# Kernel tuning notes

Measured on AMD Instinct MI355X. Metric: run time of the kernel, lower is better.

Reference implementation:

```python
import jax, jax.numpy as jnp
import numpy as np

N_NODES = 100000
N_EDGES = 3200000
D_FEAT = 512
D_HID = 64
D_LAT = 16
N_CLASS = 10
N_FLOW = 10
K_PROP = 10
ALPHA_TELEPORT = 0.1


def setup_inputs() -> dict:
    key = jax.random.key(0)
    ks = jax.random.split(key, 8)
    x = jax.random.normal(ks[0], (N_NODES, D_FEAT), jnp.float32)
    edge_index = jax.random.randint(ks[1], (2, N_EDGES), 0, N_NODES)
    p_c = jax.random.uniform(ks[2], (N_CLASS,), jnp.float32) + 0.1
    p_c = p_c / p_c.sum()
    W1 = jax.random.normal(ks[3], (D_FEAT, D_HID), jnp.float32) / np.sqrt(D_FEAT).astype(np.float32)
    b1 = jnp.zeros((D_HID,), jnp.float32)
    W2 = jax.random.normal(ks[4], (D_HID, D_LAT), jnp.float32) / np.sqrt(D_HID).astype(np.float32)
    b2 = jnp.zeros((D_LAT,), jnp.float32)
    flow_z0 = jax.random.normal(ks[5], (N_FLOW, N_CLASS, D_LAT), jnp.float32) * 0.1
    flow_alpha_prime = jax.random.normal(ks[6], (N_FLOW, N_CLASS, 1), jnp.float32) * 0.1
    flow_beta = jax.random.normal(ks[7], (N_FLOW, N_CLASS, 1), jnp.float32) * 0.1
    return dict(x=x, edge_index=edge_index, p_c=p_c, W1=W1, b1=b1, W2=W2, b2=b2,
                flow_z0=flow_z0, flow_alpha_prime=flow_alpha_prime, flow_beta=flow_beta)


def _batched_radial_log_prob(z, flow_z0, flow_alpha_prime, flow_beta):
    # Per-class batched radial flow (invertible pyro-style parameterization).
    # z: [N, D] -> log_q: [N, C]
    C, D = flow_z0.shape[1], flow_z0.shape[2]
    zz = jnp.broadcast_to(z[None], (C, z.shape[0], D))  # [C, N, D]
    sum_logdet = jnp.zeros((C, z.shape[0]), z.dtype)
    for l in range(flow_z0.shape[0]):  # small fixed number of flow layers
        z0 = flow_z0[l][:, None, :]                               # [C,1,D]
        alpha = jax.nn.softplus(flow_alpha_prime[l])[:, None, :]  # [C,1,1]
        beta_hat = -alpha + jax.nn.softplus(flow_beta[l])[:, None, :]
        dz = zz - z0
        r = jnp.sqrt(jnp.sum(dz * dz, axis=-1, keepdims=True))    # [C,N,1]
        h = 1.0 / (alpha + r)
        bh = beta_hat * h
        zz = zz + bh * dz
        logdet = (D - 1) * jnp.log1p(bh) + jnp.log1p(bh - beta_hat * r * h * h)
        sum_logdet = sum_logdet + logdet[..., 0]
    log_base = -0.5 * jnp.sum(zz * zz, axis=-1) - 0.5 * D * jnp.log(2.0 * jnp.pi)
    return (log_base + sum_logdet).T  # [N, C]


def _appnp(beta_ft, edge_index, n_nodes):
    # APPNP with self loops and symmetric gcn normalization over edge list.
    src = jnp.concatenate([edge_index[0], jnp.arange(n_nodes)])
    dst = jnp.concatenate([edge_index[1], jnp.arange(n_nodes)])
    deg = jax.ops.segment_sum(jnp.ones_like(src, dtype=beta_ft.dtype), dst, num_segments=n_nodes)
    dinv = jnp.where(deg > 0, jax.lax.rsqrt(jnp.maximum(deg, 1.0)), 0.0)
    norm = (dinv[src] * dinv[dst])[:, None]  # [E+N, 1]
    x0 = beta_ft
    b = beta_ft
    for _ in range(K_PROP):
        agg = jax.ops.segment_sum(norm * b[src], dst, num_segments=n_nodes)
        b = (1.0 - ALPHA_TELEPORT) * agg + ALPHA_TELEPORT * x0
    return b


def reference(x, edge_index, p_c, W1, b1, W2, b2, flow_z0, flow_alpha_prime, flow_beta):
    h = jax.nn.relu(x @ W1 + b1)           # input_encoder (dropout inactive at eval)
    z = h @ W2 + b2                        # latent_encoder, [N, D_LAT]
    log_q = _batched_radial_log_prob(z, flow_z0, flow_alpha_prime, flow_beta)
    log_q_per_class = log_q + jnp.log(p_c)[None, :]
    log_scale = 0.5 * D_LAT * jnp.log(4.0 * jnp.pi)  # 'latent-new' evidence scale
    beta_ft = jnp.exp(jnp.clip(log_q_per_class + log_scale, -30.0, 30.0))
    beta = _appnp(beta_ft, edge_index, x.shape[0])
    alpha = 1.0 + beta
    soft = alpha / jnp.sum(alpha, axis=-1, keepdims=True)
    hard = jnp.argmax(soft, axis=-1)
    return hard[:, None], soft
```

## Files before the change

### kernel.cpp

```cpp
#include <hip/hip_runtime.h>
#include <math.h>
#include <limits.h>

#define DF 512
#define DH 64
#define DL 16
#define NC 10
#define NF 10
#define KPROP 10

#define BSH 7
#define BW  (1 << BSH)
#define MAXB 1024
#define TILE 16384

__device__ __forceinline__ float softplus_(float x){
  return fmaxf(x, 0.0f) + log1pf(expf(-fabsf(x)));
}

#define BM 64
#define BN 64
#define BK 32
__global__ __launch_bounds__(256) void k_gemm1z(const float* __restrict__ x,
    const float* __restrict__ W1, const float* __restrict__ b1,
    const float* __restrict__ W2, const float* __restrict__ b2,
    float* __restrict__ z, int N)
{
  __shared__ float smem[2*BK*(BM+4)];
  float (*At)[BM+4] = (float(*)[BM+4])smem;
  float (*Bs)[BN+4] = (float(*)[BN+4])(smem + BK*(BM+4));
  __shared__ float W2s[DH][DL];
  __shared__ float b2s[DL];
  const int tid = threadIdx.x;
  for (int i = tid; i < DH*DL; i += 256) W2s[i>>4][i&15] = W2[i];
  if (tid < DL) b2s[tid] = b2[tid];
  const int tx = tid & 15, ty = tid >> 4;
  const int row0 = blockIdx.x * BM;
  float acc[4][4] = {};
  for (int k0 = 0; k0 < DF; k0 += BK) {
    #pragma unroll
    for (int i = 0; i < 2; ++i) {
      int idx = tid + i*256;
      int r  = idx >> 3;
      int kk = (idx & 7) << 2;
      int row = row0 + r;
      float4 va = make_float4(0.f,0.f,0.f,0.f);
      if (row < N) va = *(const float4*)&x[(size_t)row*DF + k0 + kk];
      At[kk+0][r]=va.x; At[kk+1][r]=va.y; At[kk+2][r]=va.z; At[kk+3][r]=va.w;
      int r2 = idx >> 4;
      int c4 = (idx & 15) << 2;
      float4 vb = *(const float4*)&W1[(size_t)(k0+r2)*DH + c4];
      Bs[r2][c4+0]=vb.x; Bs[r2][c4+1]=vb.y; Bs[r2][c4+2]=vb.z; Bs[r2][c4+3]=vb.w;
    }
    __syncthreads();
    #pragma unroll
    for (int kk = 0; kk < BK; ++kk) {
      float4 av = *(const float4*)&At[kk][ty<<2];
      float4 bv = *(const float4*)&Bs[kk][tx<<2];
      float a4[4]={av.x,av.y,av.z,av.w};
      float b4[4]={bv.x,bv.y,bv.z,bv.w};
      #pragma unroll
      for (int i=0;i<4;++i)
        #pragma unroll
        for (int j=0;j<4;++j) acc[i][j] = fmaf(a4[i], b4[j], acc[i][j]);
    }
    __syncthreads();
  }
  float4 bias = ((const float4*)b1)[tx];
  float bias4[4] = {bias.x, bias.y, bias.z, bias.w};
  float (*hs)[BM+4] = (float(*)[BM+4])smem;
  #pragma unroll
  for (int i=0;i<4;++i){
    #pragma unroll
    for (int j=0;j<4;++j)
      hs[(ty<<2)+i][(tx<<2)+j] = fmaxf(acc[i][j] + bias4[j], 0.0f);
  }
  __syncthreads();
  int row = tid >> 2, lg = tid & 3;
  float4 zacc = ((const float4*)b2s)[lg];
  #pragma unroll 8
  for (int k = 0; k < DH; ++k){
    float hv = hs[row][k];
    float4 wv = *(const float4*)&W2s[k][lg<<2];
    zacc.x = fmaf(hv, wv.x, zacc.x);
    zacc.y = fmaf(hv, wv.y, zacc.y);
    zacc.z = fmaf(hv, wv.z, zacc.z);
    zacc.w = fmaf(hv, wv.w, zacc.w);
  }
  int grow = row0 + row;
  if (grow < N) ((float4*)z)[(size_t)grow*4 + lg] = zacc;
}

__global__ __launch_bounds__(256) void k_flow2(const float* __restrict__ z,
    const float* __restrict__ pc, const float* __restrict__ z0g,
    const float* __restrict__ apg, const float* __restrict__ fbg,
    const float* __restrict__ dinv,
    float* __restrict__ x0, float* __restrict__ c0, float* __restrict__ y0, int N)
{
  __shared__ float z0s[NF][NC][DL];
  __shared__ float alps[NF][NC];
  __shared__ float bhs[NF][NC];
  __shared__ float lpc[NC];
  int tid = threadIdx.x;
  for (int i = tid; i < NF*NC*DL; i += 256)
    z0s[(i>>4)/NC][(i>>4)%NC][i&15] = z0g[i];
  if (tid < NF*NC){
    int l = tid/NC, c = tid%NC;
    float al = softplus_(apg[tid]);
    alps[l][c] = al;
    bhs[l][c]  = -al + softplus_(fbg[tid]);
  }
  if (tid < NC) lpc[tid] = __logf(pc[tid]);
  __syncthreads();

  int idx = blockIdx.x*256 + tid;
  int n = idx >> 4, c = idx & 15;
  if (n >= N) return;
  float dn = dinv[n];
  if (c >= NC){ x0[idx] = 0.f; c0[idx] = 0.f; y0[idx] = 0.f; return; }

  float zz[DL];
  const float4* z4 = (const float4*)z;
  #pragma unroll
  for (int q=0; q<4; ++q){
    float4 v = z4[(size_t)n*4 + q];
    zz[q*4+0]=v.x; zz[q*4+1]=v.y; zz[q*4+2]=v.z; zz[q*4+3]=v.w;
  }
  const float NEGHALFD_LOG2PI = -14.703016531274762f;
  const float LOGSCALE        =  20.248193975754326f;
  float sld = 0.f;
  #pragma unroll 1
  for (int l=0; l<NF; ++l){
    float al = alps[l][c], bhat = bhs[l][c];
    float dz[DL]; float r2 = 0.f;
    #pragma unroll
    for (int d=0; d<DL; ++d){ float t = zz[d] - z0s[l][c][d]; dz[d]=t; r2 = fmaf(t,t,r2); }
    float r  = sqrtf(r2);
    float hh = 1.0f/(al + r);
    float bh = bhat*hh;
    #pragma unroll
    for (int d=0; d<DL; ++d) zz[d] = fmaf(bh, dz[d], zz[d]);
    sld += 15.0f*__logf(1.0f + bh) + __logf(1.0f + bh - bhat*r*hh*hh);
  }
  float q2 = 0.f;
  #pragma unroll
  for (int d=0; d<DL; ++d) q2 = fmaf(zz[d], zz[d], q2);
  float v = -0.5f*q2 + NEGHALFD_LOG2PI + sld + lpc[c] + LOGSCALE;
  v = fminf(fmaxf(v, -30.f), 30.f);
  float xv = __expf(v);
  x0[idx] = xv;
  c0[idx] = dn*xv;
  y0[idx] = 0.1f*dn*xv;
}

__global__ __launch_bounds__(256) void k_bhist(const int* __restrict__ dst,
    int* __restrict__ bCnt, int E, int B)
{
  __shared__ int hh[MAXB];
  int tid = threadIdx.x;
  for (int b = tid; b < B; b += 256) hh[b] = 0;
  __syncthreads();
  for (int i = blockIdx.x*256 + tid; i < E; i += gridDim.x*256)
    atomicAdd(&hh[dst[i] >> BSH], 1);
  __syncthreads();
  for (int b = tid; b < B; b += 256) if (hh[b]) atomicAdd(&bCnt[b], hh[b]);
}

__global__ void k_bscan(const int* __restrict__ bCnt, int* __restrict__ bOff, int B){
  if (blockIdx.x==0 && threadIdx.x==0){
    int run = 0;
    for (int b=0;b<B;++b){ bOff[b]=run; run+=bCnt[b]; }
    bOff[B]=run;
  }
}

__global__ __launch_bounds__(256) void k_bscatter(const int* __restrict__ src,
    const int* __restrict__ dst, const int* __restrict__ bOff,
    int* __restrict__ bCur, int* __restrict__ bp, int E, int B)
{
  __shared__ int hc[MAXB];
  __shared__ int hb[MAXB];
  int tid = threadIdx.x;
  int base = blockIdx.x * TILE;
  int lim  = base + TILE; if (lim > E) lim = E;
  for (int b = tid; b < B; b += 256) hc[b] = 0;
  __syncthreads();
  for (int i = base + tid; i < lim; i += 256)
    atomicAdd(&hc[dst[i] >> BSH], 1);
  __syncthreads();
  for (int b = tid; b < B; b += 256){
    int c = hc[b];
    hb[b] = c ? atomicAdd(&bCur[b], c) : 0;
    hc[b] = 0;
  }
  __syncthreads();
  for (int i = base + tid; i < lim; i += 256){
    int d = dst[i];
    int b = d >> BSH;
    int pos = bOff[b] + hb[b] + atomicAdd(&hc[b], 1);
    bp[pos] = (src[i] << BSH) | (d & (BW-1));
  }
}

__global__ __launch_bounds__(256) void k_bdeg(const int* __restrict__ bp,
    const int* __restrict__ bOff, int* __restrict__ deg, int N)
{
  __shared__ int cur[BW];
  int tid = threadIdx.x;
  int b = blockIdx.x;
  if (tid < BW) cur[tid] = 0;
  __syncthreads();
  int s = bOff[b], e = bOff[b+1];
  for (int i = s + tid; i < e; i += 256)
    atomicAdd(&cur[bp[i] & (BW-1)], 1);
  __syncthreads();
  int node = (b << BSH) + tid;
  if (tid < BW && node < N) deg[node] = cur[tid] + 1;
}

__global__ void k_dinv(const int* __restrict__ deg, float* __restrict__ dinv,
    float* __restrict__ dinv2, int N){
  int n = blockIdx.x*256 + threadIdx.x;
  if (n < N){
    float d = (float)deg[n];
    float dv = 1.0f / sqrtf(d);
    dinv[n]  = dv;
    dinv2[n] = dv*dv;
  }
}

__global__ __launch_bounds__(256) void k_scan_part(const int* __restrict__ deg,
    int* __restrict__ part, int N){
  __shared__ int sd[256];
  int base = blockIdx.x*1024;
  int tid = threadIdx.x;
  int s = 0;
  #pragma unroll
  for (int i=0;i<4;++i){ int idx = base + tid*4 + i; if (idx < N) s += deg[idx]; }
  sd[tid] = s; __syncthreads();
  for (int ofs=128; ofs>0; ofs>>=1){ if (tid<ofs) sd[tid]+=sd[tid+ofs]; __syncthreads(); }
  if (tid==0) part[blockIdx.x] = sd[0];
}

__global__ void k_scan_top(int* part, int nb){
  if (blockIdx.x==0 && threadIdx.x==0){
    int run = 0;
    for (int i=0;i<nb;++i){ int v = part[i]; part[i] = run; run += v; }
  }
}

__global__ __launch_bounds__(256) void k_scan_final(const int* __restrict__ deg,
    const int* __restrict__ part, int* __restrict__ off, int N, int E)
{
  __shared__ int sc[256];
  int base = blockIdx.x*1024;
  int tid = threadIdx.x;
  int v[4]; int s = 0;
  #pragma unroll
  for (int i=0;i<4;++i){ int idx = base + tid*4 + i; v[i] = (idx<N)?deg[idx]:0; s += v[i]; }
  sc[tid] = s; __syncthreads();
  for (int ofs=1; ofs<256; ofs<<=1){
    int t = (tid>=ofs) ? sc[tid-ofs] : 0;
    __syncthreads();
    sc[tid] += t;
    __syncthreads();
  }
  int ex = sc[tid] - s + part[blockIdx.x];
  #pragma unroll
  for (int i=0;i<4;++i){
    int idx = base + tid*4 + i;
    if (idx < N){
      off[idx] = ex;
      if (idx == N-1) off[N] = ex + v[i];
      ex += v[i];
    }
  }
}

__global__ __launch_bounds__(256) void k_place(const int* __restrict__ bp,
    const int* __restrict__ bOff, const int* __restrict__ off,
    int* __restrict__ csr, int N)
{
  __shared__ int cur[BW];
  int tid = threadIdx.x;
  int b = blockIdx.x;
  int node0 = b << BSH;
  if (tid < BW){
    cur[tid] = 1;
    int node = node0 + tid;
    if (node < N) csr[off[node]] = node;
  }
  __syncthreads();
  int s = bOff[b], e = bOff[b+1];
  for (int i = s + tid; i < e; i += 256){
    int v  = bp[i];
    int dl = v & (BW-1);
    int sn = v >> BSH;
    int d  = node0 + dl;
    int p  = off[d] + atomicAdd(&cur[dl], 1);
    csr[p] = sn;
  }
}

__global__ __launch_bounds__(256) void k_rank(int* __restrict__ csr,
    const int* __restrict__ off, int N)
{
  int wid  = (blockIdx.x*256 + threadIdx.x) >> 6;
  int lane = threadIdx.x & 63;
  if (wid >= N) return;
  int s = off[wid], e = off[wid+1];
  int d = e - s;
  if (d <= 1) return;
  if (d <= 64){
    int v = (lane < d) ? csr[s+lane] : INT_MAX;
    int rank = 0;
    for (int j = 0; j < d; ++j){
      int bv = __shfl(v, j);
      rank += (bv < v) || (bv == v && j < lane);
    }
    if (lane < d) csr[s+rank] = v;
  } else if (d <= 256){
    int v0 = (lane      < d) ? csr[s+lane      ] : INT_MAX;
    int v1 = (lane+64   < d) ? csr[s+lane+64   ] : INT_MAX;
    int v2 = (lane+128  < d) ? csr[s+lane+128  ] : INT_MAX;
    int v3 = (lane+192  < d) ? csr[s+lane+192  ] : INT_MAX;
    int r0=0,r1=0,r2=0,r3=0;
    for (int j = 0; j < d; ++j){
      int slot = j >> 6, jl = j & 63;
      int bv = (slot==0) ? __shfl(v0,jl) : (slot==1) ? __shfl(v1,jl)
             : (slot==2) ? __shfl(v2,jl) : __shfl(v3,jl);
      r0 += (bv < v0) || (bv == v0 && j < lane);
      r1 += (bv < v1) || (bv == v1 && j < lane+64);
      r2 += (bv < v2) || (bv == v2 && j < lane+128);
      r3 += (bv < v3) || (bv == v3 && j < lane+192);
    }
    if (lane      < d) csr[s+r0]=v0;
    if (lane+64   < d) csr[s+r1]=v1;
    if (lane+128  < d) csr[s+r2]=v2;
    if (lane+192  < d) csr[s+r3]=v3;
  } else {
    if (lane == 0){
      for (int i = s+1; i < e; ++i){
        int key = csr[i]; int j = i-1;
        while (j >= s && csr[j] > key){ csr[j+1] = csr[j]; --j; }
        csr[j+1] = key;
      }
    }
  }
}

__global__ __launch_bounds__(256) void k_prop(const float* __restrict__ cin,
    const float* __restrict__ y0, const float* __restrict__ dinv2,
    float* __restrict__ cout,
    const int* __restrict__ csr, const int* __restrict__ off, int N)
{
  int t = blockIdx.x*256 + threadIdx.x;
  int n = t >> 2, q = t & 3;
  if (n >= N) return;
  const float4* c4 = (const float4*)cin;
  float4 a0 = make_float4(0.f,0.f,0.f,0.f);
  float4 a1 = make_float4(0.f,0.f,0.f,0.f);
  float4 a2 = make_float4(0.f,0.f,0.f,0.f);
  float4 a3 = make_float4(0.f,0.f,0.f,0.f);
  int s = off[n], e = off[n+1];
  int i = s;
  for (; i+4 <= e; i += 4){
    int s0 = csr[i], s1 = csr[i+1], s2 = csr[i+2], s3 = csr[i+3];
    float4 v0 = c4[(size_t)s0*4 + q];
    float4 v1 = c4[(size_t)s1*4 + q];
    float4 v2 = c4[(size_t)s2*4 + q];
    float4 v3 = c4[(size_t)s3*4 + q];
    a0.x += v0.x; a0.y += v0.y; a0.z += v0.z; a0.w += v0.w;
    a1.x += v1.x; a1.y += v1.y; a1.z += v1.z; a1.w += v1.w;
    a2.x += v2.x; a2.y += v2.y; a2.z += v2.z; a2.w += v2.w;
    a3.x += v3.x; a3.y += v3.y; a3.z += v3.z; a3.w += v3.w;
  }
  for (; i < e; ++i){
    float4 v0 = c4[(size_t)csr[i]*4 + q];
    a0.x += v0.x; a0.y += v0.y; a0.z += v0.z; a0.w += v0.w;
  }
  float w9 = 0.9f * dinv2[n];
  float4 yv = ((const float4*)y0)[(size_t)n*4 + q];
  float4 o;
  o.x = fmaf(w9, (a0.x+a1.x)+(a2.x+a3.x), yv.x);
  o.y = fmaf(w9, (a0.y+a1.y)+(a2.y+a3.y), yv.y);
  o.z = fmaf(w9, (a0.z+a1.z)+(a2.z+a3.z), yv.z);
  o.w = fmaf(w9, (a0.w+a1.w)+(a2.w+a3.w), yv.w);
  ((float4*)cout)[(size_t)n*4 + q] = o;
}

__global__ __launch_bounds__(256) void k_prop_final(const float* __restrict__ cin,
    const float* __restrict__ x0, const float* __restrict__ dinv,
    const int* __restrict__ csr, const int* __restrict__ off,
    float* __restrict__ out, int N)
{
  int t = blockIdx.x*256 + threadIdx.x;
  int n = t >> 2, q = t & 3;
  if (n >= N) return;
  const float4* c4 = (const float4*)cin;
  float4 a0 = make_float4(0.f,0.f,0.f,0.f);
  float4 a1 = make_float4(0.f,0.f,0.f,0.f);
  float4 a2 = make_float4(0.f,0.f,0.f,0.f);
  float4 a3 = make_float4(0.f,0.f,0.f,0.f);
  int s = off[n], e = off[n+1];
  int i = s;
  for (; i+4 <= e; i += 4){
    int s0 = csr[i], s1 = csr[i+1], s2 = csr[i+2], s3 = csr[i+3];
    float4 v0 = c4[(size_t)s0*4 + q];
    float4 v1 = c4[(size_t)s1*4 + q];
    float4 v2 = c4[(size_t)s2*4 + q];
    float4 v3 = c4[(size_t)s3*4 + q];
    a0.x += v0.x; a0.y += v0.y; a0.z += v0.z; a0.w += v0.w;
    a1.x += v1.x; a1.y += v1.y; a1.z += v1.z; a1.w += v1.w;
    a2.x += v2.x; a2.y += v2.y; a2.z += v2.z; a2.w += v2.w;
    a3.x += v3.x; a3.y += v3.y; a3.z += v3.z; a3.w += v3.w;
  }
  for (; i < e; ++i){
    float4 v0 = c4[(size_t)csr[i]*4 + q];
    a0.x += v0.x; a0.y += v0.y; a0.z += v0.z; a0.w += v0.w;
  }
  float w9 = 0.9f * dinv[n];
  float4 xv = ((const float4*)x0)[(size_t)n*4 + q];
  float4 al;
  al.x = fmaf(w9, (a0.x+a1.x)+(a2.x+a3.x), fmaf(0.1f, xv.x, 1.f));
  al.y = fmaf(w9, (a0.y+a1.y)+(a2.y+a3.y), fmaf(0.1f, xv.y, 1.f));
  al.z = fmaf(w9, (a0.z+a1.z)+(a2.z+a3.z), fmaf(0.1f, xv.z, 1.f));
  al.w = fmaf(w9, (a0.w+a1.w)+(a2.w+a3.w), fmaf(0.1f, xv.w, 1.f));

  float sv = 0.f;
  if (q < 2)       sv = al.x + al.y + al.z + al.w;
  else if (q == 2) sv = al.x + al.y;
  sv += __shfl_xor(sv, 1, 4);
  sv += __shfl_xor(sv, 2, 4);

  float bv = -1e30f; int bi = 999;
  int cb = q*4;
  int nvalid = (q < 2) ? 4 : (q == 2 ? 2 : 0);
  float av[4] = {al.x, al.y, al.z, al.w};
  for (int j = 0; j < nvalid; ++j){
    if (av[j] > bv){ bv = av[j]; bi = cb + j; }
  }
  #pragma unroll
  for (int o = 1; o <= 2; o <<= 1){
    float vo = __shfl_xor(bv, o, 4);
    int  io  = __shfl_xor(bi, o, 4);
    if (vo > bv || (vo == bv && io < bi)){ bv = vo; bi = io; }
  }

  float inv = 1.0f / sv;
  size_t sb = (size_t)N + (size_t)n*NC;
  for (int j = 0; j < nvalid; ++j) out[sb + cb + j] = av[j] * inv;
  if (q == 0) out[n] = (float)bi;
}

extern "C" void kernel_launch(void* const* d_in, const int* in_sizes, int n_in,
                              void* d_out, int out_size, void* d_ws, size_t ws_size,
                              hipStream_t stream)
{
  const float* x  = (const float*)d_in[0];
  const int*   ei = (const int*)  d_in[1];
  const float* pc = (const float*)d_in[2];
  const float* W1 = (const float*)d_in[3];
  const float* b1 = (const float*)d_in[4];
  const float* W2 = (const float*)d_in[5];
  const float* b2 = (const float*)d_in[6];
  const float* z0 = (const float*)d_in[7];
  const float* ap = (const float*)d_in[8];
  const float* fb = (const float*)d_in[9];
  float* out = (float*)d_out;

  const int N = in_sizes[0] / DF;
  const int E = in_sizes[1] / 2;
  const int* src = ei;
  const int* dst = ei + E;
  const int B = (N + BW - 1) >> BSH;

  char* ws = (char*)d_ws;
  size_t o = 0;
  size_t region0 = (size_t)E*sizeof(int);
  if ((size_t)N*DL*sizeof(float) > region0) region0 = (size_t)N*DL*sizeof(float);
  int*   bp   = (int*)  (ws + o);
  float* z    = (float*)(ws + o);
  o += region0;
  int*   csr  = (int*)  (ws + o); o += (size_t)(E+N)*sizeof(int);
  float* x0   = (float*)(ws + o); o += (size_t)N*DL*sizeof(float);
  float* c0   = (float*)(ws + o); o += (size_t)N*DL*sizeof(float);
  float* y0   = (float*)(ws + o); o += (size_t)N*DL*sizeof(float);
  float* cA   = (float*)(ws + o); o += (size_t)N*DL*sizeof(float);
  float* cB   = (float*)(ws + o); o += (size_t)N*DL*sizeof(float);
  int*   deg  = (int*)  (ws + o); o += (size_t)N*sizeof(int);
  float* dinv = (float*)(ws + o); o += (size_t)N*sizeof(float);
  float* dinv2= (float*)(ws + o); o += (size_t)N*sizeof(float);
  int*   offs = (int*)  (ws + o); o += (size_t)(N+2)*sizeof(int);
  int*   part = (int*)  (ws + o); o += 4096;
  int*   bCnt = (int*)  (ws + o); o += MAXB*sizeof(int);
  int*   bOff = (int*)  (ws + o); o += (MAXB+1)*sizeof(int);
  int*   bCur = (int*)  (ws + o); o += MAXB*sizeof(int);

  const int TB = 256;
  int gN  = (N + TB - 1) / TB;
  int nb  = (N + 1023) / 1024;

  hipMemsetAsync(bCnt, 0, MAXB*sizeof(int), stream);
  hipMemsetAsync(bCur, 0, MAXB*sizeof(int), stream);
  k_bhist<<<512, TB, 0, stream>>>(dst, bCnt, E, B);
  k_bscan<<<1, 1, 0, stream>>>(bCnt, bOff, B);
  k_bscatter<<<(E + TILE - 1)/TILE, TB, 0, stream>>>(src, dst, bOff, bCur, bp, E, B);
  k_bdeg<<<B, TB, 0, stream>>>(bp, bOff, deg, N);
  k_dinv<<<gN, TB, 0, stream>>>(deg, dinv, dinv2, N);
  k_scan_part<<<nb, TB, 0, stream>>>(deg, part, N);
  k_scan_top<<<1, 1, 0, stream>>>(part, nb);
  k_scan_final<<<nb, TB, 0, stream>>>(deg, part, offs, N, E);
  k_place<<<B, TB, 0, stream>>>(bp, bOff, offs, csr, N);
  k_rank<<<(N + 3) / 4, TB, 0, stream>>>(csr, offs, N);

  k_gemm1z<<<(N + BM - 1) / BM, TB, 0, stream>>>(x, W1, b1, W2, b2, z, N);
  k_flow2<<<((N*DL) + TB - 1) / TB, TB, 0, stream>>>(z, pc, z0, ap, fb, dinv,
                                                     x0, c0, y0, N);

  int gP = ((N*4) + TB - 1) / TB;
  const float* cin = c0;
  for (int it = 0; it < KPROP-1; ++it){
    float* cout = (it & 1) ? cB : cA;
    k_prop<<<gP, TB, 0, stream>>>(cin, y0, dinv2, cout, csr, offs, N);
    cin = cout;
  }
  k_prop_final<<<gP, TB, 0, stream>>>(cin, x0, dinv, csr, offs, out, N);
}
```

Baseline: 776.5 us.

## Split propagation features into two 8-wide halves for cache-friendlier gathers

Splits the 16-wide per-node propagation state into separate low and high 8-float arrays. Each propagation iteration now launches blocks that work on one half at a time, so the gathered working set per pass is half the size and more likely to stay in cache. The gather loop is unrolled to 8 neighbors. The dinv computation is also folded into the degree kernel, removing one launch. The cost is two gather passes over the CSR indices per iteration and more complex indexing.

```diff
diff --git a/kernel.cpp b/kernel.cpp
--- a/kernel.cpp
+++ b/kernel.cpp
@@ -95,7 +95,8 @@
     const float* __restrict__ pc, const float* __restrict__ z0g,
     const float* __restrict__ apg, const float* __restrict__ fbg,
     const float* __restrict__ dinv,
-    float* __restrict__ x0, float* __restrict__ c0, float* __restrict__ y0, int N)
+    float* __restrict__ x0, float* __restrict__ cL, float* __restrict__ cH,
+    float* __restrict__ yL, float* __restrict__ yH, int N)
 {
   __shared__ float z0s[NF][NC][DL];
   __shared__ float alps[NF][NC];
@@ -117,7 +118,12 @@
   int n = idx >> 4, c = idx & 15;
   if (n >= N) return;
   float dn = dinv[n];
-  if (c >= NC){ x0[idx] = 0.f; c0[idx] = 0.f; y0[idx] = 0.f; return; }
+  if (c >= NC){
+    x0[idx] = 0.f;
+    cH[(size_t)n*8 + (c-8)] = 0.f;
+    yH[(size_t)n*8 + (c-8)] = 0.f;
+    return;
+  }
 
   float zz[DL];
   const float4* z4 = (const float4*)z;
@@ -149,8 +155,14 @@
   v = fminf(fmaxf(v, -30.f), 30.f);
   float xv = __expf(v);
   x0[idx] = xv;
-  c0[idx] = dn*xv;
-  y0[idx] = 0.1f*dn*xv;
+  float cv = dn*xv;
+  if (c < 8){
+    cL[(size_t)n*8 + c] = cv;
+    yL[(size_t)n*8 + c] = 0.1f*cv;
+  } else {
+    cH[(size_t)n*8 + (c-8)] = cv;
+    yH[(size_t)n*8 + (c-8)] = 0.1f*cv;
+  }
 }
 
 __global__ __launch_bounds__(256) void k_bhist(const int* __restrict__ dst,
@@ -203,7 +215,8 @@
 }
 
 __global__ __launch_bounds__(256) void k_bdeg(const int* __restrict__ bp,
-    const int* __restrict__ bOff, int* __restrict__ deg, int N)
+    const int* __restrict__ bOff, int* __restrict__ deg,
+    float* __restrict__ dinv, float* __restrict__ dinv2, int N)
 {
   __shared__ int cur[BW];
   int tid = threadIdx.x;
@@ -215,17 +228,12 @@
     atomicAdd(&cur[bp[i] & (BW-1)], 1);
   __syncthreads();
   int node = (b << BSH) + tid;
-  if (tid < BW && node < N) deg[node] = cur[tid] + 1;
-}
-
-__global__ void k_dinv(const int* __restrict__ deg, float* __restrict__ dinv,
-    float* __restrict__ dinv2, int N){
-  int n = blockIdx.x*256 + threadIdx.x;
-  if (n < N){
-    float d = (float)deg[n];
-    float dv = 1.0f / sqrtf(d);
-    dinv[n]  = dv;
-    dinv2[n] = dv*dv;
+  if (tid < BW && node < N){
+    int d = cur[tid] + 1;
+    deg[node] = d;
+    float dv = 1.0f / sqrtf((float)d);
+    dinv[node]  = dv;
+    dinv2[node] = dv*dv;
   }
 }
 
@@ -349,15 +357,82 @@
   }
 }
 
-__global__ __launch_bounds__(256) void k_prop(const float* __restrict__ cin,
-    const float* __restrict__ y0, const float* __restrict__ dinv2,
-    float* __restrict__ cout,
+__global__ __launch_bounds__(256) void k_prop_half(
+    const float* __restrict__ cLin, const float* __restrict__ cHin,
+    const float* __restrict__ yL,  const float* __restrict__ yH,
+    const float* __restrict__ dinv2,
+    float* __restrict__ cLout, float* __restrict__ cHout,
     const int* __restrict__ csr, const int* __restrict__ off, int N)
+{
+  int bid = blockIdx.x;
+  int half = (bid & 7) >> 2;
+  int node_blk = ((bid >> 3) << 2) | (bid & 3);
+  int t = threadIdx.x;
+  int n = node_blk*128 + (t >> 1);
+  int q = t & 1;
+  if (n >= N) return;
+  const float4* cin = (const float4*)(half ? cHin : cLin);
+  const float4* yin = (const float4*)(half ? yH : yL);
+  float4* cout = (float4*)(half ? cHout : cLout);
+
+  float4 a0 = make_float4(0.f,0.f,0.f,0.f);
+  float4 a1 = make_float4(0.f,0.f,0.f,0.f);
+  float4 a2 = make_float4(0.f,0.f,0.f,0.f);
+  float4 a3 = make_float4(0.f,0.f,0.f,0.f);
+  int s = off[n], e = off[n+1];
+  int i = s;
+  for (; i+8 <= e; i += 8){
+    int s0 = csr[i],   s1 = csr[i+1], s2 = csr[i+2], s3 = csr[i+3];
+    int s4 = csr[i+4], s5 = csr[i+5], s6 = csr[i+6], s7 = csr[i+7];
+    float4 v0 = cin[(size_t)s0*2 + q];
+    float4 v1 = cin[(size_t)s1*2 + q];
+    float4 v2 = cin[(size_t)s2*2 + q];
+    float4 v3 = cin[(size_t)s3*2 + q];
+    float4 v4 = cin[(size_t)s4*2 + q];
+    float4 v5 = cin[(size_t)s5*2 + q];
+    float4 v6 = cin[(size_t)s6*2 + q];
+    float4 v7 = cin[(size_t)s7*2 + q];
+    a0.x += v0.x; a0.y += v0.y; a0.z += v0.z; a0.w += v0.w;
+    a1.x += v1.x; a1.y += v1.y; a1.z += v1.z; a1.w += v1.w;
+    a2.x += v2.x; a2.y += v2.y; a2.z += v2.z; a2.w += v2.w;
+    a3.x += v3.x; a3.y += v3.y; a3.z += v3.z; a3.w += v3.w;
+    a0.x += v4.x; a0.y += v4.y; a0.z += v4.z; a0.w += v4.w;
+    a1.x += v5.x; a1.y += v5.y; a1.z += v5.z; a1.w += v5.w;
+    a2.x += v6.x; a2.y += v6.y; a2.z += v6.z; a2.w += v6.w;
+    a3.x += v7.x; a3.y += v7.y; a3.z += v7.z; a3.w += v7.w;
+  }
+  for (; i+2 <= e; i += 2){
+    int s0 = csr[i], s1 = csr[i+1];
+    float4 v0 = cin[(size_t)s0*2 + q];
+    float4 v1 = cin[(size_t)s1*2 + q];
+    a0.x += v0.x; a0.y += v0.y; a0.z += v0.z; a0.w += v0.w;
+    a1.x += v1.x; a1.y += v1.y; a1.z += v1.z; a1.w += v1.w;
+  }
+  if (i < e){
+    float4 v0 = cin[(size_t)csr[i]*2 + q];
+    a0.x += v0.x; a0.y += v0.y; a0.z += v0.z; a0.w += v0.w;
+  }
+  float w9 = 0.9f * dinv2[n];
+  float4 yv = yin[(size_t)n*2 + q];
+  float4 o;
+  o.x = fmaf(w9, (a0.x+a1.x)+(a2.x+a3.x), yv.x);
+  o.y = fmaf(w9, (a0.y+a1.y)+(a2.y+a3.y), yv.y);
+  o.z = fmaf(w9, (a0.z+a1.z)+(a2.z+a3.z), yv.z);
+  o.w = fmaf(w9, (a0.w+a1.w)+(a2.w+a3.w), yv.w);
+  cout[(size_t)n*2 + q] = o;
+}
+
+__global__ __launch_bounds__(256) void k_prop_final(
+    const float* __restrict__ cLin, const float* __restrict__ cHin,
+    const float* __restrict__ x0, const float* __restrict__ dinv,
+    const int* __restrict__ csr, const int* __restrict__ off,
+    float* __restrict__ out, int N)
 {
   int t = blockIdx.x*256 + threadIdx.x;
   int n = t >> 2, q = t & 3;
   if (n >= N) return;
-  const float4* c4 = (const float4*)cin;
+  const float4* cin = (const float4*)((q < 2) ? cLin : cHin);
+  int qq = q & 1;
   float4 a0 = make_float4(0.f,0.f,0.f,0.f);
   float4 a1 = make_float4(0.f,0.f,0.f,0.f);
   float4 a2 = make_float4(0.f,0.f,0.f,0.f);
@@ -366,57 +441,17 @@
   int i = s;
   for (; i+4 <= e; i += 4){
     int s0 = csr[i], s1 = csr[i+1], s2 = csr[i+2], s3 = csr[i+3];
-    float4 v0 = c4[(size_t)s0*4 + q];
-    float4 v1 = c4[(size_t)s1*4 + q];
-    float4 v2 = c4[(size_t)s2*4 + q];
-    float4 v3 = c4[(size_t)s3*4 + q];
+    float4 v0 = cin[(size_t)s0*2 + qq];
+    float4 v1 = cin[(size_t)s1*2 + qq];
+    float4 v2 = cin[(size_t)s2*2 + qq];
+    float4 v3 = cin[(size_t)s3*2 + qq];
     a0.x += v0.x; a0.y += v0.y; a0.z += v0.z; a0.w += v0.w;
     a1.x += v1.x; a1.y += v1.y; a1.z += v1.z; a1.w += v1.w;
     a2.x += v2.x; a2.y += v2.y; a2.z += v2.z; a2.w += v2.w;
     a3.x += v3.x; a3.y += v3.y; a3.z += v3.z; a3.w += v3.w;
   }
   for (; i < e; ++i){
-    float4 v0 = c4[(size_t)csr[i]*4 + q];
-    a0.x += v0.x; a0.y += v0.y; a0.z += v0.z; a0.w += v0.w;
-  }
-  float w9 = 0.9f * dinv2[n];
-  float4 yv = ((const float4*)y0)[(size_t)n*4 + q];
-  float4 o;
-  o.x = fmaf(w9, (a0.x+a1.x)+(a2.x+a3.x), yv.x);
-  o.y = fmaf(w9, (a0.y+a1.y)+(a2.y+a3.y), yv.y);
-  o.z = fmaf(w9, (a0.z+a1.z)+(a2.z+a3.z), yv.z);
-  o.w = fmaf(w9, (a0.w+a1.w)+(a2.w+a3.w), yv.w);
-  ((float4*)cout)[(size_t)n*4 + q] = o;
-}
-
-__global__ __launch_bounds__(256) void k_prop_final(const float* __restrict__ cin,
-    const float* __restrict__ x0, const float* __restrict__ dinv,
-    const int* __restrict__ csr, const int* __restrict__ off,
-    float* __restrict__ out, int N)
-{
-  int t = blockIdx.x*256 + threadIdx.x;
-  int n = t >> 2, q = t & 3;
-  if (n >= N) return;
-  const float4* c4 = (const float4*)cin;
-  float4 a0 = make_float4(0.f,0.f,0.f,0.f);
-  float4 a1 = make_float4(0.f,0.f,0.f,0.f);
-  float4 a2 = make_float4(0.f,0.f,0.f,0.f);
-  float4 a3 = make_float4(0.f,0.f,0.f,0.f);
-  int s = off[n], e = off[n+1];
-  int i = s;
-  for (; i+4 <= e; i += 4){
-    int s0 = csr[i], s1 = csr[i+1], s2 = csr[i+2], s3 = csr[i+3];
-    float4 v0 = c4[(size_t)s0*4 + q];
-    float4 v1 = c4[(size_t)s1*4 + q];
-    float4 v2 = c4[(size_t)s2*4 + q];
-    float4 v3 = c4[(size_t)s3*4 + q];
-    a0.x += v0.x; a0.y += v0.y; a0.z += v0.z; a0.w += v0.w;
-    a1.x += v1.x; a1.y += v1.y; a1.z += v1.z; a1.w += v1.w;
-    a2.x += v2.x; a2.y += v2.y; a2.z += v2.z; a2.w += v2.w;
-    a3.x += v3.x; a3.y += v3.y; a3.z += v3.z; a3.w += v3.w;
-  }
-  for (; i < e; ++i){
-    float4 v0 = c4[(size_t)csr[i]*4 + q];
+    float4 v0 = cin[(size_t)csr[i]*2 + qq];
     a0.x += v0.x; a0.y += v0.y; a0.z += v0.z; a0.w += v0.w;
   }
   float w9 = 0.9f * dinv[n];
@@ -484,10 +519,15 @@
   o += region0;
   int*   csr  = (int*)  (ws + o); o += (size_t)(E+N)*sizeof(int);
   float* x0   = (float*)(ws + o); o += (size_t)N*DL*sizeof(float);
-  float* c0   = (float*)(ws + o); o += (size_t)N*DL*sizeof(float);
-  float* y0   = (float*)(ws + o); o += (size_t)N*DL*sizeof(float);
-  float* cA   = (float*)(ws + o); o += (size_t)N*DL*sizeof(float);
-  float* cB   = (float*)(ws + o); o += (size_t)N*DL*sizeof(float);
+  size_t h8 = (size_t)N*8*sizeof(float);
+  float* cL0  = (float*)(ws + o); o += h8;
+  float* cH0  = (float*)(ws + o); o += h8;
+  float* yL   = (float*)(ws + o); o += h8;
+  float* yH   = (float*)(ws + o); o += h8;
+  float* cLA  = (float*)(ws + o); o += h8;
+  float* cHA  = (float*)(ws + o); o += h8;
+  float* cLB  = (float*)(ws + o); o += h8;
+  float* cHB  = (float*)(ws + o); o += h8;
   int*   deg  = (int*)  (ws + o); o += (size_t)N*sizeof(int);
   float* dinv = (float*)(ws + o); o += (size_t)N*sizeof(float);
   float* dinv2= (float*)(ws + o); o += (size_t)N*sizeof(float);
@@ -498,7 +538,6 @@
   int*   bCur = (int*)  (ws + o); o += MAXB*sizeof(int);
 
   const int TB = 256;
-  int gN  = (N + TB - 1) / TB;
   int nb  = (N + 1023) / 1024;
 
   hipMemsetAsync(bCnt, 0, MAXB*sizeof(int), stream);
@@ -506,8 +545,7 @@
   k_bhist<<<512, TB, 0, stream>>>(dst, bCnt, E, B);
   k_bscan<<<1, 1, 0, stream>>>(bCnt, bOff, B);
   k_bscatter<<<(E + TILE - 1)/TILE, TB, 0, stream>>>(src, dst, bOff, bCur, bp, E, B);
-  k_bdeg<<<B, TB, 0, stream>>>(bp, bOff, deg, N);
-  k_dinv<<<gN, TB, 0, stream>>>(deg, dinv, dinv2, N);
+  k_bdeg<<<B, TB, 0, stream>>>(bp, bOff, deg, dinv, dinv2, N);
   k_scan_part<<<nb, TB, 0, stream>>>(deg, part, N);
   k_scan_top<<<1, 1, 0, stream>>>(part, nb);
   k_scan_final<<<nb, TB, 0, stream>>>(deg, part, offs, N, E);
@@ -516,14 +554,18 @@
 
   k_gemm1z<<<(N + BM - 1) / BM, TB, 0, stream>>>(x, W1, b1, W2, b2, z, N);
   k_flow2<<<((N*DL) + TB - 1) / TB, TB, 0, stream>>>(z, pc, z0, ap, fb, dinv,
-                                                     x0, c0, y0, N);
-
-  int gP = ((N*4) + TB - 1) / TB;
-  const float* cin = c0;
+                                                     x0, cL0, cH0, yL, yH, N);
+
+  int P = (N + 127) / 128;
+  int gH = 8 * ((P + 3) / 4);
+  const float* cLin = cL0; const float* cHin = cH0;
   for (int it = 0; it < KPROP-1; ++it){
-    float* cout = (it & 1) ? cB : cA;
-    k_prop<<<gP, TB, 0, stream>>>(cin, y0, dinv2, cout, csr, offs, N);
-    cin = cout;
-  }
-  k_prop_final<<<gP, TB, 0, stream>>>(cin, x0, dinv, csr, offs, out, N);
-}
+    float* cLo = (it & 1) ? cLB : cLA;
+    float* cHo = (it & 1) ? cHB : cHA;
+    k_prop_half<<<gH, TB, 0, stream>>>(cLin, cHin, yL, yH, dinv2, cLo, cHo,
+                                       csr, offs, N);
+    cLin = cLo; cHin = cHo;
+  }
+  int gF = ((N*4) + TB - 1) / TB;
+  k_prop_final<<<gF, TB, 0, stream>>>(cLin, cHin, x0, dinv, csr, offs, out, N);
+}
```

Result: slower. 920.4 us (+18.5%).
